# Kernel optimization log

Hardware: AMD Instinct MI355X
Metric: run time of the kernel (lower is better)

## Reference

```python
import jax, jax.numpy as jnp
import numpy as np

NUM_BLOCKS = 10  # labels 1..10; label 0 = background
EPS = 1e-6


def setup_inputs() -> dict:
    key = jax.random.key(0)
    k1, k2, k3 = jax.random.split(key, 3)
    shape = (8, 128, 128, 128)
    inp = jax.random.uniform(k1, shape, dtype=jnp.float32)
    tgt = jax.random.uniform(k2, shape, dtype=jnp.float32)
    blk = jax.random.randint(k3, shape, 0, NUM_BLOCKS + 1, dtype=jnp.int32)
    return {"input": inp, "target": tgt, "block": blk}


def _dice_from_sums(intersect, input_area, target_area):
    # intersect/areas: [B, NUM_BLOCKS]; faithful to cal_dice_loss per block.
    denom = input_area + target_area + 2.0 * EPS
    batch_loss = 1.0 - 2.0 * intersect / denom          # [B, NUM_BLOCKS]
    batch_loss = jnp.where(target_area == 0, 0.0, batch_loss)
    valid = jnp.sum(target_area != 0, axis=0).astype(batch_loss.dtype)  # [NUM_BLOCKS]
    return jnp.sum(batch_loss, axis=0) / jnp.maximum(valid, 1.0)        # [NUM_BLOCKS]


def reference(input, target, block):
    B = input.shape[0]
    x = input.reshape(B, -1)
    t = target.reshape(B, -1)
    s = block.reshape(B, -1)

    # One fused pass: per-batch segmented sums over block ids 0..NUM_BLOCKS.
    seg = jax.vmap(lambda v, ids: jax.ops.segment_sum(v, ids, num_segments=NUM_BLOCKS + 1))
    intersect = seg(x * t, s)[:, 1:]   # [B, 10] sum(input*target) within each block
    input_area = seg(x, s)[:, 1:]      # [B, 10]
    target_area = seg(t, s)[:, 1:]     # [B, 10]

    loss_per_block = _dice_from_sums(intersect, input_area, target_area)  # [10]

    # block_tmp.max() != 0  <=>  label b+1 appears anywhere in the tensor
    counts = jnp.sum(s[..., None] == jnp.arange(1, NUM_BLOCKS + 1), axis=(0, 1))
    present = counts > 0                                                   # [10]
    num = jnp.sum(present).astype(loss_per_block.dtype)
    loss = jnp.sum(jnp.where(present, loss_per_block, 0.0)) / num
    return (loss, 0)
```

## Files before the change

### kernel.cpp

```cpp
#include <hip/hip_runtime.h>

#define NB 10
#define BATCH 8
#define EPSF 1e-6f

constexpr int THREADS        = 256;
constexpr int VEC_PER_BATCH  = (128 * 128 * 128) / 4;
constexpr int BLOCKS_PER_BATCH = 64;
constexpr int GRID           = BLOCKS_PER_BATCH * BATCH;
constexpr int WAVE_VEC       = 2048;
constexpr int STAGES         = WAVE_VEC / 64;
constexpr int RING           = 4;


__device__ __forceinline__ void dma16(const void* g, void* l) {
    __builtin_amdgcn_global_load_lds(
        (const __attribute__((address_space(1))) void*)g,
        (__attribute__((address_space(3))) void*)l, 16, 0, 0);
}

__global__ __launch_bounds__(THREADS)
void dice_partial(const float* __restrict__ x,
                  const float* __restrict__ t,
                  const int*   __restrict__ s,
                  float* __restrict__ ws)
{
    __shared__ float4 lx[4][RING][64];
    __shared__ float4 lt[4][RING][64];
    __shared__ int4   lsb[4][RING][64];

    const int tid  = threadIdx.x;
    const int wave = tid >> 6, lane = tid & 63;
    const int batch = blockIdx.x >> 6;
    const int sub   = blockIdx.x & 63;
    const long long chunk = (long long)batch * VEC_PER_BATCH
                          + (long long)(sub * 4 + wave) * WAVE_VEC;

    const float4* gx = (const float4*)x + chunk + lane;
    const float4* gt = (const float4*)t + chunk + lane;
    const int4*   gs = (const int4*)s  + chunk + lane;

    float aI[NB], aX[NB], aT[NB];
#pragma unroll
    for (int k = 0; k < NB; ++k) { aI[k] = 0.f; aX[k] = 0.f; aT[k] = 0.f; }
    unsigned bits = 0;

#define DO_ELEM(xe, te, se)                                     \
    do {                                                        \
        const float _x = (xe), _t = (te);                       \
        const int   _s = (se);                                  \
        const float _p = _x * _t;                               \
        bits |= (1u << _s);                                     \
        _Pragma("unroll")                                       \
        for (int k = 0; k < NB; ++k) {                          \
            const float m = (_s == k + 1) ? 1.0f : 0.0f;        \
            aI[k] = fmaf(m, _p, aI[k]);                         \
            aX[k] = fmaf(m, _x, aX[k]);                         \
            aT[k] = fmaf(m, _t, aT[k]);                         \
        }                                                       \
    } while (0)

#pragma unroll
    for (int i = 0; i < 3; ++i) {
        dma16(gx + i * 64, &lx[wave][i][0]);
        dma16(gt + i * 64, &lt[wave][i][0]);
        dma16(gs + i * 64, &lsb[wave][i][0]);
    }
    const float4* px = gx + 3 * 64;
    const float4* pt = gt + 3 * 64;
    const int4*   ps = gs + 3 * 64;

#pragma unroll 1
    for (int i = 0; i < STAGES; ++i) {
        if (i < STAGES - 3) {
            const int nb = (i + 3) & 3;
            dma16(px, &lx[wave][nb][0]);
            dma16(pt, &lt[wave][nb][0]);
            dma16(ps, &lsb[wave][nb][0]);
            px += 64; pt += 64; ps += 64;
        }
        if (i < STAGES - 3)       asm volatile("s_waitcnt vmcnt(9)" ::: "memory");
        else if (i == STAGES - 3) asm volatile("s_waitcnt vmcnt(6)" ::: "memory");
        else if (i == STAGES - 2) asm volatile("s_waitcnt vmcnt(3)" ::: "memory");
        else                      asm volatile("s_waitcnt vmcnt(0)" ::: "memory");
        __builtin_amdgcn_sched_barrier(0);

        const int b = i & 3;
        const float4 xv = lx[wave][b][lane];
        const float4 tv = lt[wave][b][lane];
        const int4   sv = lsb[wave][b][lane];
        DO_ELEM(xv.x, tv.x, sv.x);
        DO_ELEM(xv.y, tv.y, sv.y);
        DO_ELEM(xv.z, tv.z, sv.z);
        DO_ELEM(xv.w, tv.w, sv.w);
    }
#undef DO_ELEM

#pragma unroll
    for (int k = 0; k < NB; ++k) {
#pragma unroll
        for (int off = 32; off > 0; off >>= 1) {
            aI[k] += __shfl_xor(aI[k], off);
            aX[k] += __shfl_xor(aX[k], off);
            aT[k] += __shfl_xor(aT[k], off);
        }
    }
#pragma unroll
    for (int off = 32; off > 0; off >>= 1)
        bits |= (unsigned)__shfl_xor((int)bits, off);

    __shared__ float    wsum[4][32];
    __shared__ unsigned wb[4];
    if (lane < NB) {
        wsum[wave][lane]          = aI[lane];
        wsum[wave][NB + lane]     = aX[lane];
        wsum[wave][2 * NB + lane] = aT[lane];
    }
    if (lane == 0) wb[wave] = bits;
    __syncthreads();

    if (tid < 3 * NB) {
        const float v = wsum[0][tid] + wsum[1][tid] + wsum[2][tid] + wsum[3][tid];
        ws[tid * GRID + blockIdx.x] = v;
    }
    if (tid == 0)
        ((unsigned*)ws)[3 * NB * GRID + blockIdx.x] = wb[0] | wb[1] | wb[2] | wb[3];
}

__global__ void dice_final(const float* __restrict__ ws, float* __restrict__ out)
{
    const int tid = threadIdx.x;
    __shared__ float    sums[BATCH * 3 * NB];
    __shared__ unsigned um[THREADS];

    const int grp = tid >> 4, l16 = tid & 15;
#pragma unroll
    for (int j = 0; j < 15; ++j) {
        const int c = grp + 16 * j;
        const int batch = c / (3 * NB);
        const int idx   = c % (3 * NB);
        const float4 v4 = *(const float4*)&ws[idx * GRID + batch * BLOCKS_PER_BATCH + l16 * 4];
        float v = v4.x + v4.y + v4.z + v4.w;
        v += __shfl_xor(v, 8);
        v += __shfl_xor(v, 4);
        v += __shfl_xor(v, 2);
        v += __shfl_xor(v, 1);
        if (l16 == 0) sums[c] = v;
    }

    const unsigned* mrow = (const unsigned*)ws + 3 * NB * GRID;
    um[tid] = mrow[tid] | mrow[tid + 256];
    __syncthreads();
    for (int st = THREADS / 2; st > 0; st >>= 1) {
        if (tid < st) um[tid] |= um[tid + st];
        __syncthreads();
    }
    const unsigned mask = um[0];

    if (tid < 64) {
        float lpb = 0.0f, pres = 0.0f;
        if (tid < NB) {
            float sum_loss = 0.0f, valid = 0.0f;
            for (int b = 0; b < BATCH; ++b) {
                const float I = sums[b * 3 * NB + tid];
                const float X = sums[b * 3 * NB + NB + tid];
                const float T = sums[b * 3 * NB + 2 * NB + tid];
                const float denom = X + T + 2.0f * EPSF;
                float bl = 1.0f - 2.0f * I / denom;
                if (T == 0.0f) bl = 0.0f; else valid += 1.0f;
                sum_loss += bl;
            }
            lpb  = sum_loss / fmaxf(valid, 1.0f);
            pres = ((mask >> (tid + 1)) & 1u) ? 1.0f : 0.0f;
        }
        float num = pres;
        float ls  = (pres > 0.0f) ? lpb : 0.0f;
#pragma unroll
        for (int off = 32; off > 0; off >>= 1) {
            num += __shfl_down(num, off);
            ls  += __shfl_down(ls,  off);
        }
        if (tid == 0) {
            out[0] = ls / num;
            out[1] = 0.0f;
        }
    }
}

extern "C" void kernel_launch(void* const* d_in, const int* in_sizes, int n_in,
                              void* d_out, int out_size, void* d_ws, size_t ws_size,
                              hipStream_t stream)
{
    const float* x = (const float*)d_in[0];
    const float* t = (const float*)d_in[1];
    const int*   s = (const int*)d_in[2];
    float* out = (float*)d_out;
    float* ws  = (float*)d_ws;

    dice_partial<<<GRID, THREADS, 0, stream>>>(x, t, s, ws);
    dice_final<<<1, THREADS, 0, stream>>>(ws, out);
}
```

Before: 50.60 us.

## Raise grid to 96 blocks per batch with uneven stage split and earlier waits

Grows the grid from 64 to 96 blocks per batch (768 blocks total), so the work spreads across more CUs on MI355X. Each wave now gets an uneven number of 64-vector stages, with the remainder handed out to the first waves. The prefetch loop is reordered to wait first and then issue the next load with a vmcnt(6) threshold, which may reduce how many loads are in flight. The final kernel is adapted to the new partial count, using scalar strided reads and a third mask row.

Result: no change. 50.70 us (+0.2%).

```diff
diff --git a/kernel.cpp b/kernel.cpp
--- a/kernel.cpp
+++ b/kernel.cpp
@@ -4,13 +4,14 @@
 #define BATCH 8
 #define EPSF 1e-6f
 
-constexpr int THREADS        = 256;
-constexpr int VEC_PER_BATCH  = (128 * 128 * 128) / 4;
-constexpr int BLOCKS_PER_BATCH = 64;
-constexpr int GRID           = BLOCKS_PER_BATCH * BATCH;
-constexpr int WAVE_VEC       = 2048;
-constexpr int STAGES         = WAVE_VEC / 64;
-constexpr int RING           = 4;
+constexpr int THREADS          = 256;
+constexpr int VEC_PER_BATCH    = (128 * 128 * 128) / 4;
+constexpr int BLOCKS_PER_BATCH = 96;
+constexpr int GRID             = BLOCKS_PER_BATCH * BATCH;
+constexpr int WAVES_PER_BATCH  = BLOCKS_PER_BATCH * 4;
+constexpr int ST_PER_BATCH     = VEC_PER_BATCH / 64;
+constexpr int STQ              = ST_PER_BATCH / WAVES_PER_BATCH;
+constexpr int STR              = ST_PER_BATCH - STQ * WAVES_PER_BATCH;
 
 
 __device__ __forceinline__ void dma16(const void* g, void* l) {
@@ -25,20 +26,22 @@
                   const int*   __restrict__ s,
                   float* __restrict__ ws)
 {
-    __shared__ float4 lx[4][RING][64];
-    __shared__ float4 lt[4][RING][64];
-    __shared__ int4   lsb[4][RING][64];
+    __shared__ float4 lx[4][4][64];
+    __shared__ float4 lt[4][4][64];
+    __shared__ int4   lsb[4][4][64];
 
     const int tid  = threadIdx.x;
     const int wave = tid >> 6, lane = tid & 63;
-    const int batch = blockIdx.x >> 6;
-    const int sub   = blockIdx.x & 63;
-    const long long chunk = (long long)batch * VEC_PER_BATCH
-                          + (long long)(sub * 4 + wave) * WAVE_VEC;
-
-    const float4* gx = (const float4*)x + chunk + lane;
-    const float4* gt = (const float4*)t + chunk + lane;
-    const int4*   gs = (const int4*)s  + chunk + lane;
+    const int batch = blockIdx.x / BLOCKS_PER_BATCH;
+    const int sub   = blockIdx.x % BLOCKS_PER_BATCH;
+    const int wb    = sub * 4 + wave;
+    const int NSTG  = STQ + (wb < STR ? 1 : 0);
+    const long long start = (long long)batch * VEC_PER_BATCH
+                          + ((long long)wb * STQ + (wb < STR ? wb : STR)) * 64 + lane;
+
+    const float4* gx = (const float4*)x + start;
+    const float4* gt = (const float4*)t + start;
+    const int4*   gs = (const int4*)s  + start;
 
     float aI[NB], aX[NB], aT[NB];
 #pragma unroll
@@ -71,19 +74,19 @@
     const int4*   ps = gs + 3 * 64;
 
 #pragma unroll 1
-    for (int i = 0; i < STAGES; ++i) {
-        if (i < STAGES - 3) {
+    for (int i = 0; i < NSTG; ++i) {
+        if (i < NSTG - 2)       asm volatile("s_waitcnt vmcnt(6)" ::: "memory");
+        else if (i == NSTG - 2) asm volatile("s_waitcnt vmcnt(3)" ::: "memory");
+        else                    asm volatile("s_waitcnt vmcnt(0)" ::: "memory");
+        __builtin_amdgcn_sched_barrier(0);
+
+        if (i + 3 < NSTG) {
             const int nb = (i + 3) & 3;
             dma16(px, &lx[wave][nb][0]);
             dma16(pt, &lt[wave][nb][0]);
             dma16(ps, &lsb[wave][nb][0]);
             px += 64; pt += 64; ps += 64;
         }
-        if (i < STAGES - 3)       asm volatile("s_waitcnt vmcnt(9)" ::: "memory");
-        else if (i == STAGES - 3) asm volatile("s_waitcnt vmcnt(6)" ::: "memory");
-        else if (i == STAGES - 2) asm volatile("s_waitcnt vmcnt(3)" ::: "memory");
-        else                      asm volatile("s_waitcnt vmcnt(0)" ::: "memory");
-        __builtin_amdgcn_sched_barrier(0);
 
         const int b = i & 3;
         const float4 xv = lx[wave][b][lane];
@@ -110,13 +113,13 @@
         bits |= (unsigned)__shfl_xor((int)bits, off);
 
     __shared__ float    wsum[4][32];
-    __shared__ unsigned wb[4];
+    __shared__ unsigned wbm[4];
     if (lane < NB) {
         wsum[wave][lane]          = aI[lane];
         wsum[wave][NB + lane]     = aX[lane];
         wsum[wave][2 * NB + lane] = aT[lane];
     }
-    if (lane == 0) wb[wave] = bits;
+    if (lane == 0) wbm[wave] = bits;
     __syncthreads();
 
     if (tid < 3 * NB) {
@@ -124,7 +127,7 @@
         ws[tid * GRID + blockIdx.x] = v;
     }
     if (tid == 0)
-        ((unsigned*)ws)[3 * NB * GRID + blockIdx.x] = wb[0] | wb[1] | wb[2] | wb[3];
+        ((unsigned*)ws)[3 * NB * GRID + blockIdx.x] = wbm[0] | wbm[1] | wbm[2] | wbm[3];
 }
 
 __global__ void dice_final(const float* __restrict__ ws, float* __restrict__ out)
@@ -139,8 +142,11 @@
         const int c = grp + 16 * j;
         const int batch = c / (3 * NB);
         const int idx   = c % (3 * NB);
-        const float4 v4 = *(const float4*)&ws[idx * GRID + batch * BLOCKS_PER_BATCH + l16 * 4];
-        float v = v4.x + v4.y + v4.z + v4.w;
+        const int base  = idx * GRID + batch * BLOCKS_PER_BATCH;
+        float v = 0.0f;
+#pragma unroll
+        for (int q = 0; q < BLOCKS_PER_BATCH / 16; ++q)
+            v += ws[base + q * 16 + l16];
         v += __shfl_xor(v, 8);
         v += __shfl_xor(v, 4);
         v += __shfl_xor(v, 2);
@@ -149,7 +155,7 @@
     }
 
     const unsigned* mrow = (const unsigned*)ws + 3 * NB * GRID;
-    um[tid] = mrow[tid] | mrow[tid + 256];
+    um[tid] = mrow[tid] | mrow[tid + 256] | mrow[tid + 512];
     __syncthreads();
     for (int st = THREADS / 2; st > 0; st >>= 1) {
         if (tid < st) um[tid] |= um[tid + st];
```

## Fuse final reduction into partial kernel via last-block atomic counter

Applied to the files above, without the earlier changes.

Merges the two-kernel reduction into one kernel: each block writes its partials, then increments a global counter, and the last block to arrive performs the final dice computation. This removes the second kernel launch and the gap between launches, but adds a memset of the counter, threadfences and an atomic. It also moves the waitcnt ahead of the DMA issue in the load loop, which changes how many loads are in flight per stage.

New measurement: 101.5 us. 101% more time.

```diff
diff --git a/kernel.cpp b/kernel.cpp
--- a/kernel.cpp
+++ b/kernel.cpp
@@ -4,14 +4,14 @@
 #define BATCH 8
 #define EPSF 1e-6f
 
-constexpr int THREADS        = 256;
-constexpr int VEC_PER_BATCH  = (128 * 128 * 128) / 4;
+constexpr int THREADS          = 256;
+constexpr int VEC_PER_BATCH    = (128 * 128 * 128) / 4;
 constexpr int BLOCKS_PER_BATCH = 64;
-constexpr int GRID           = BLOCKS_PER_BATCH * BATCH;
-constexpr int WAVE_VEC       = 2048;
-constexpr int STAGES         = WAVE_VEC / 64;
-constexpr int RING           = 4;
-
+constexpr int GRID             = BLOCKS_PER_BATCH * BATCH;
+constexpr int WAVE_VEC         = 2048;
+constexpr int STAGES           = WAVE_VEC / 64;
+
+constexpr int CTR_OFF = 31 * GRID;
 
 __device__ __forceinline__ void dma16(const void* g, void* l) {
     __builtin_amdgcn_global_load_lds(
@@ -20,14 +20,16 @@
 }
 
 __global__ __launch_bounds__(THREADS)
-void dice_partial(const float* __restrict__ x,
-                  const float* __restrict__ t,
-                  const int*   __restrict__ s,
-                  float* __restrict__ ws)
+void dice_fused(const float* __restrict__ x,
+                const float* __restrict__ t,
+                const int*   __restrict__ s,
+                float* __restrict__ ws,
+                float* __restrict__ out,
+                unsigned* __restrict__ ctr)
 {
-    __shared__ float4 lx[4][RING][64];
-    __shared__ float4 lt[4][RING][64];
-    __shared__ int4   lsb[4][RING][64];
+    __shared__ float4 lx[4][4][64];
+    __shared__ float4 lt[4][4][64];
+    __shared__ int4   lsb[4][4][64];
 
     const int tid  = threadIdx.x;
     const int wave = tid >> 6, lane = tid & 63;
@@ -72,6 +74,11 @@
 
 #pragma unroll 1
     for (int i = 0; i < STAGES; ++i) {
+        if (i <= STAGES - 3)      asm volatile("s_waitcnt vmcnt(6)" ::: "memory");
+        else if (i == STAGES - 2) asm volatile("s_waitcnt vmcnt(3)" ::: "memory");
+        else                      asm volatile("s_waitcnt vmcnt(0)" ::: "memory");
+        __builtin_amdgcn_sched_barrier(0);
+
         if (i < STAGES - 3) {
             const int nb = (i + 3) & 3;
             dma16(px, &lx[wave][nb][0]);
@@ -79,11 +86,6 @@
             dma16(ps, &lsb[wave][nb][0]);
             px += 64; pt += 64; ps += 64;
         }
-        if (i < STAGES - 3)       asm volatile("s_waitcnt vmcnt(9)" ::: "memory");
-        else if (i == STAGES - 3) asm volatile("s_waitcnt vmcnt(6)" ::: "memory");
-        else if (i == STAGES - 2) asm volatile("s_waitcnt vmcnt(3)" ::: "memory");
-        else                      asm volatile("s_waitcnt vmcnt(0)" ::: "memory");
-        __builtin_amdgcn_sched_barrier(0);
 
         const int b = i & 3;
         const float4 xv = lx[wave][b][lane];
@@ -110,13 +112,13 @@
         bits |= (unsigned)__shfl_xor((int)bits, off);
 
     __shared__ float    wsum[4][32];
-    __shared__ unsigned wb[4];
+    __shared__ unsigned wbm[4];
     if (lane < NB) {
         wsum[wave][lane]          = aI[lane];
         wsum[wave][NB + lane]     = aX[lane];
         wsum[wave][2 * NB + lane] = aT[lane];
     }
-    if (lane == 0) wb[wave] = bits;
+    if (lane == 0) wbm[wave] = bits;
     __syncthreads();
 
     if (tid < 3 * NB) {
@@ -124,12 +126,16 @@
         ws[tid * GRID + blockIdx.x] = v;
     }
     if (tid == 0)
-        ((unsigned*)ws)[3 * NB * GRID + blockIdx.x] = wb[0] | wb[1] | wb[2] | wb[3];
-}
-
-__global__ void dice_final(const float* __restrict__ ws, float* __restrict__ out)
-{
-    const int tid = threadIdx.x;
+        ((unsigned*)ws)[3 * NB * GRID + blockIdx.x] = wbm[0] | wbm[1] | wbm[2] | wbm[3];
+
+    __threadfence();
+    __syncthreads();
+    __shared__ unsigned amLast;
+    if (tid == 0) amLast = (atomicAdd(ctr, 1u) == GRID - 1);
+    __syncthreads();
+    if (!amLast) return;
+    __threadfence();
+
     __shared__ float    sums[BATCH * 3 * NB];
     __shared__ unsigned um[THREADS];
 
@@ -137,9 +143,9 @@
 #pragma unroll
     for (int j = 0; j < 15; ++j) {
         const int c = grp + 16 * j;
-        const int batch = c / (3 * NB);
-        const int idx   = c % (3 * NB);
-        const float4 v4 = *(const float4*)&ws[idx * GRID + batch * BLOCKS_PER_BATCH + l16 * 4];
+        const int bb  = c / (3 * NB);
+        const int idx = c % (3 * NB);
+        const float4 v4 = *(const float4*)&ws[idx * GRID + bb * BLOCKS_PER_BATCH + l16 * 4];
         float v = v4.x + v4.y + v4.z + v4.w;
         v += __shfl_xor(v, 8);
         v += __shfl_xor(v, 4);
@@ -196,7 +202,8 @@
     const int*   s = (const int*)d_in[2];
     float* out = (float*)d_out;
     float* ws  = (float*)d_ws;
-
-    dice_partial<<<GRID, THREADS, 0, stream>>>(x, t, s, ws);
-    dice_final<<<1, THREADS, 0, stream>>>(ws, out);
+    unsigned* ctr = (unsigned*)ws + CTR_OFF;
+
+    hipMemsetAsync(ctr, 0, sizeof(unsigned), stream);
+    dice_fused<<<GRID, THREADS, 0, stream>>>(x, t, s, ws, out, ctr);
 }
```
